# Kernel optimization log

Hardware: AMD Instinct MI355X
Metric: run time of the kernel (lower is better)

Reference implementation:

```python
import jax, jax.numpy as jnp
import numpy as np

B, N, NC, D, DC, L, NH = 8, 512, 256, 512, 256, 12, 8
DK = D // NH


def _ln(x, g, b, eps=1e-5):
    m = x.mean(-1, keepdims=True)
    v = ((x - m) ** 2).mean(-1, keepdims=True)
    return (x - m) * jax.lax.rsqrt(v + eps) * g + b


def setup_inputs() -> dict:
    key = jax.random.key(0)
    ks = iter(jax.random.split(key, 64))
    def rn(shape, s=1.0):
        return jax.random.normal(next(ks), shape, dtype=jnp.float32) * s
    w = 0.02
    inp = {
        "x_t": rn((B, N, 2)),
        "a_t": jax.random.uniform(next(ks), (B, N, N), dtype=jnp.float32),
        "hdse_node": rn((B, N, D), 0.1),
        "hdse_bias": rn((B, NH, N, N), 0.1),
        "context": rn((B, NC, DC)),
        "coord_w": rn((2, D), w), "coord_b": jnp.zeros((D,)),
        "deg_w": rn((1, D), w), "deg_b": jnp.zeros((D,)),
        "tm_w1": rn((D, 4 * D), w), "tm_b1": jnp.zeros((4 * D,)),
        "tm_w2": rn((4 * D, D), w), "tm_b2": jnp.zeros((D,)),
        "ln_sa_g": jnp.ones((L, D)), "ln_sa_b": jnp.zeros((L, D)),
        "qkv_w": rn((L, D, 3 * D), w), "qkv_b": jnp.zeros((L, 3 * D)),
        "osa_w": rn((L, D, D), w), "osa_b": jnp.zeros((L, D)),
        "ln_ca_g": jnp.ones((L, D)), "ln_ca_b": jnp.zeros((L, D)),
        "qca_w": rn((L, D, D), w), "qca_b": jnp.zeros((L, D)),
        "kvca_w": rn((L, DC, 2 * D), w), "kvca_b": jnp.zeros((L, 2 * D)),
        "oca_w": rn((L, D, D), w), "oca_b": jnp.zeros((L, D)),
        "ln_ff_g": jnp.ones((L, D)), "ln_ff_b": jnp.zeros((L, D)),
        "ff1_w": rn((L, D, 4 * D), w), "ff1_b": jnp.zeros((L, 4 * D)),
        "ff2_w": rn((L, 4 * D, D), w), "ff2_b": jnp.zeros((L, D)),
        "fn_g": jnp.ones((D,)), "fn_b": jnp.zeros((D,)),
        "ch_w": rn((D, 2), w), "ch_b": jnp.zeros((2,)),
        "es_w": rn((D, D // 4), w), "es_b": jnp.zeros((D // 4,)),
        "ed_w": rn((D, D // 4), w), "ed_b": jnp.zeros((D // 4,)),
        "eb": jnp.zeros((1,)),
        "t": jax.random.randint(next(ks), (B,), 0, 1000),
        "node_mask": jnp.ones((B, N), dtype=bool),
        "context_mask": jnp.ones((B, NC), dtype=bool),
    }
    return inp


def reference(x_t, a_t, hdse_node, hdse_bias, context,
              coord_w, coord_b, deg_w, deg_b,
              tm_w1, tm_b1, tm_w2, tm_b2,
              ln_sa_g, ln_sa_b, qkv_w, qkv_b, osa_w, osa_b,
              ln_ca_g, ln_ca_b, qca_w, qca_b, kvca_w, kvca_b, oca_w, oca_b,
              ln_ff_g, ln_ff_b, ff1_w, ff1_b, ff2_w, ff2_b,
              fn_g, fn_b, ch_w, ch_b, es_w, es_b, ed_w, ed_b, eb,
              t, node_mask, context_mask):
    scale = 1.0 / np.sqrt(DK).astype(np.float32)
    # input embedding: coords + degree + timestep + HDSE node encodings
    h = x_t @ coord_w + coord_b
    h = h + a_t.sum(-1, keepdims=True) @ deg_w + deg_b
    half = D // 2
    freqs = jnp.exp(-jnp.log(10000.0) * jnp.arange(half, dtype=jnp.float32) / half)
    ang = t.astype(jnp.float32)[:, None] * freqs[None, :]
    emb = jnp.concatenate([jnp.sin(ang), jnp.cos(ang)], -1)
    temb = jax.nn.gelu(emb @ tm_w1 + tm_b1, approximate=False) @ tm_w2 + tm_b2
    h = h + temb[:, None, :] + hdse_node
    nmask = node_mask[:, None, None, :]
    cmask = context_mask[:, None, None, :]
    for i in range(L):
        # self-attention with HDSE bias
        hn = _ln(h, ln_sa_g[i], ln_sa_b[i])
        qkv = (hn @ qkv_w[i] + qkv_b[i]).reshape(B, N, 3, NH, DK)
        q, k, v = [jnp.moveaxis(qkv[:, :, j], 1, 2) for j in range(3)]  # (B,NH,N,DK)
        s = jnp.einsum('bhnd,bhmd->bhnm', q, k) * scale + hdse_bias
        s = jnp.where(nmask, s, -1e9)
        sa = jnp.einsum('bhnm,bhmd->bhnd', jax.nn.softmax(s, -1), v)
        sa = jnp.moveaxis(sa, 1, 2).reshape(B, N, D)
        h = h + sa @ osa_w[i] + osa_b[i]
        # cross-attention to context
        hn = _ln(h, ln_ca_g[i], ln_ca_b[i])
        q = jnp.moveaxis((hn @ qca_w[i] + qca_b[i]).reshape(B, N, NH, DK), 1, 2)
        kv = (context @ kvca_w[i] + kvca_b[i]).reshape(B, NC, 2, NH, DK)
        kc = jnp.moveaxis(kv[:, :, 0], 1, 2)
        vc = jnp.moveaxis(kv[:, :, 1], 1, 2)
        s = jnp.einsum('bhnd,bhmd->bhnm', q, kc) * scale
        s = jnp.where(cmask, s, -1e9)
        ca = jnp.einsum('bhnm,bhmd->bhnd', jax.nn.softmax(s, -1), vc)
        ca = jnp.moveaxis(ca, 1, 2).reshape(B, N, D)
        h = h + ca @ oca_w[i] + oca_b[i]
        # FFN
        hn = _ln(h, ln_ff_g[i], ln_ff_b[i])
        h = h + jax.nn.gelu(hn @ ff1_w[i] + ff1_b[i], approximate=False) @ ff2_w[i] + ff2_b[i]
    h = _ln(h, fn_g, fn_b)
    eps = h @ ch_w + ch_b
    hs = h @ es_w + es_b
    hd = h @ ed_w + ed_b
    el = jnp.einsum('bne,bme->bnm', hs, hd) + eb[0]
    el = (el + jnp.swapaxes(el, 1, 2)) * 0.5
    el = jnp.where(jnp.eye(N, dtype=bool)[None], 0.0, el)
    eps = eps * node_mask[..., None].astype(eps.dtype)
    pm = node_mask[:, :, None] & node_mask[:, None, :]
    el = jnp.where(pm, el, 0.0)
    return eps, el
```

## Files before the change

### kernel.cpp

```cpp
#include <hip/hip_runtime.h>


#define DEV static __device__ __forceinline__

typedef __attribute__((ext_vector_type(8))) short short8;
typedef __attribute__((ext_vector_type(4))) short short4v;
typedef __attribute__((ext_vector_type(4))) float f32x4;

DEV float b2f(unsigned short u) {
    union { unsigned int i; float f; } x; x.i = ((unsigned int)u) << 16; return x.f;
}
DEV unsigned short f2b(float f) {
    union { float f; unsigned int i; } x; x.f = f;
    unsigned int i = x.i;
    return (unsigned short)((i + 0x7fffu + ((i >> 16) & 1u)) >> 16);
}
DEV float gelu_exact(float x) { return 0.5f * x * (1.0f + erff(x * 0.70710678118654752440f)); }

DEV void load_lds16(const unsigned short* g, unsigned short* l) {
    __builtin_amdgcn_global_load_lds(
        (const __attribute__((address_space(1))) unsigned int*)g,
        (__attribute__((address_space(3))) unsigned int*)l, 16, 0, 0);
}

template<int BM, int BN, int EPI>
__launch_bounds__(256)
__global__ void gemm_bt(const unsigned short* __restrict__ A, int lda, long sA1, long sA2,
                        const unsigned short* __restrict__ Bt, int ldb, long sB1, long sB2,
                        void* __restrict__ Cv, int ldc, long sC1, long sC2,
                        const float* __restrict__ bias,
                        int K, int NZ2)
{
    constexpr int WM = BM / 2, WN = BN / 2;
    constexpr int MF = WM / 16, NF = WN / 16;
    constexpr int LA = BM / 64, LB = BN / 64;
    __shared__ __align__(16) unsigned short lA0[BM * 32];
    __shared__ __align__(16) unsigned short lA1[BM * 32];
    __shared__ __align__(16) unsigned short lB0[BN * 32];
    __shared__ __align__(16) unsigned short lB1[BN * 32];

    const int tid = threadIdx.x;
    const int lane = tid & 63, wave = tid >> 6;
    const int quad = lane >> 4, l16 = lane & 15;
    const int wm = wave >> 1, wn = wave & 1;

    const int z = blockIdx.z;
    const int z1 = z / NZ2, z2 = z - z1 * NZ2;
    const unsigned short* Ab = A + z1 * sA1 + z2 * sA2 + (long)blockIdx.y * BM * lda;
    const unsigned short* Bb = Bt + z1 * sB1 + z2 * sB2 + (long)blockIdx.x * BN * ldb;

    const int srow = tid >> 2, scol = (tid & 3) * 8;

    f32x4 acc[MF][NF] = {};

    auto stage = [&](unsigned short* dA, unsigned short* dB, int k0) {
        #pragma unroll
        for (int i = 0; i < LA; i++)
            load_lds16(Ab + (long)(srow + i * 64) * lda + k0 + scol,
                       dA + (srow + i * 64) * 32 + scol);
        #pragma unroll
        for (int i = 0; i < LB; i++)
            load_lds16(Bb + (long)(srow + i * 64) * ldb + k0 + scol,
                       dB + (srow + i * 64) * 32 + scol);
    };
    auto compute = [&](const unsigned short* sA, const unsigned short* sB) {
        short8 af[MF], bf[NF];
        #pragma unroll
        for (int m = 0; m < MF; m++)
            af[m] = *(const short8*)&sA[(wm * WM + m * 16 + l16) * 32 + quad * 8];
        #pragma unroll
        for (int n = 0; n < NF; n++)
            bf[n] = *(const short8*)&sB[(wn * WN + n * 16 + l16) * 32 + quad * 8];
        #pragma unroll
        for (int m = 0; m < MF; m++)
            #pragma unroll
            for (int n = 0; n < NF; n++)
                acc[m][n] = __builtin_amdgcn_mfma_f32_16x16x32_bf16(af[m], bf[n], acc[m][n], 0, 0, 0);
    };

    const int nk = K >> 5;
    stage(lA0, lB0, 0);
    __syncthreads();

    for (int t = 0; t < nk; t += 2) {
        stage(lA1, lB1, (t + 1) << 5);
        compute(lA0, lB0);
        __syncthreads();
        if (t + 2 < nk) stage(lA0, lB0, (t + 2) << 5);
        compute(lA1, lB1);
        __syncthreads();
    }

    const long cb = z1 * sC1 + z2 * sC2;
    const int r0 = blockIdx.y * BM + wm * WM + quad * 4;
    const int c0 = blockIdx.x * BN + wn * WN + l16;
    #pragma unroll
    for (int m = 0; m < MF; m++) {
        #pragma unroll
        for (int n = 0; n < NF; n++) {
            const int c = c0 + n * 16;
            float bvv = 0.f;
            if (EPI == 0 || EPI == 1 || EPI == 2) bvv = bias ? bias[c] : 0.f;
            #pragma unroll
            for (int t2 = 0; t2 < 4; t2++) {
                const int r = r0 + m * 16 + t2;
                const float v = acc[m][n][t2];
                const long idx = cb + (long)r * ldc + c;
                if (EPI == 0) {
                    ((unsigned short*)Cv)[idx] = f2b(v + bvv);
                } else if (EPI == 1) {
                    ((unsigned short*)Cv)[idx] = f2b(gelu_exact(v + bvv));
                } else if (EPI == 2) {
                    float* Cf = (float*)Cv;
                    Cf[idx] = Cf[idx] + v + bvv;
                } else {
                    ((float*)Cv)[idx] = v;
                }
            }
        }
    }
}

template<int NKT, bool HB>
__launch_bounds__(256)
__global__ void attn_fused(const unsigned short* __restrict__ Qp, int ldq,
                           const unsigned short* __restrict__ Kp, int ldk,
                           const unsigned short* __restrict__ Vt,
                           const unsigned short* __restrict__ biasp,
                           unsigned short* __restrict__ Out)
{
    constexpr int KEYS = NKT * 128;
    __shared__ __align__(16) unsigned short kbuf[8192];
    __shared__ __align__(16) unsigned short vbuf[8192];
    __shared__ __align__(16) unsigned short pbuf[8192];

    const int tid = threadIdx.x;
    const int lane = tid & 63, w = tid >> 6;
    const int quad = lane >> 4, l16 = lane & 15;
    const int qblk = blockIdx.x;
    const int bh = blockIdx.y;
    const int b = bh >> 3, hh = bh & 7;

    const unsigned short* Q = Qp + (long)(b * 512 + qblk * 64) * ldq + hh * 64;
    const unsigned short* K = Kp + (long)b * KEYS * ldk + hh * 64;
    const unsigned short* V = Vt + (long)bh * 64 * KEYS;
    const unsigned short* Bi = HB ? biasp + (long)bh * 262144 + (long)(qblk * 64) * 512 : nullptr;
    unsigned short* O = Out + (long)(b * 512 + qblk * 64) * 512 + hh * 64;

    const short8 a0 = *(const short8*)(Q + (long)(w * 16 + l16) * ldq + quad * 8);
    const short8 a1 = *(const short8*)(Q + (long)(w * 16 + l16) * ldq + 32 + quad * 8);

    f32x4 acc[NKT * 8];
    #pragma unroll
    for (int f = 0; f < NKT * 8; f++) acc[f] = f32x4{0.f, 0.f, 0.f, 0.f};

    for (int kt = 0; kt < NKT; kt++) {
        __syncthreads();
        #pragma unroll
        for (int p = 0; p < 4; p++) {
            const int key = p * 32 + (tid >> 3);
            const int col = (tid & 7) * 8;
            short8 v = *(const short8*)(K + (long)(kt * 128 + key) * ldk + col);
            *(short8*)&kbuf[(col >> 5) * 4096 + key * 32 + (col & 31)] = v;
        }
        __syncthreads();
        #pragma unroll
        for (int nf = 0; nf < 8; nf++) {
            const short8 b0 = *(const short8*)&kbuf[(nf * 16 + l16) * 32 + quad * 8];
            const short8 b1 = *(const short8*)&kbuf[4096 + (nf * 16 + l16) * 32 + quad * 8];
            acc[kt * 8 + nf] = __builtin_amdgcn_mfma_f32_16x16x32_bf16(a0, b0, acc[kt * 8 + nf], 0, 0, 0);
            acc[kt * 8 + nf] = __builtin_amdgcn_mfma_f32_16x16x32_bf16(a1, b1, acc[kt * 8 + nf], 0, 0, 0);
        }
    }

    float rmax[4] = {-1e30f, -1e30f, -1e30f, -1e30f};
    #pragma unroll
    for (int f = 0; f < NKT * 8; f++) {
        const int col = (f >> 3) * 128 + (f & 7) * 16 + l16;
        #pragma unroll
        for (int j = 0; j < 4; j++) {
            float v = acc[f][j] * 0.125f;
            if (HB) v += b2f(Bi[(long)(w * 16 + quad * 4 + j) * 512 + col]);
            acc[f][j] = v;
            rmax[j] = fmaxf(rmax[j], v);
        }
    }
    #pragma unroll
    for (int m = 1; m < 16; m <<= 1)
        #pragma unroll
        for (int j = 0; j < 4; j++) rmax[j] = fmaxf(rmax[j], __shfl_xor(rmax[j], m, 64));
    float rsum[4] = {0.f, 0.f, 0.f, 0.f};
    #pragma unroll
    for (int f = 0; f < NKT * 8; f++)
        #pragma unroll
        for (int j = 0; j < 4; j++) {
            const float e = __expf(acc[f][j] - rmax[j]);
            acc[f][j] = e;
            rsum[j] += e;
        }
    #pragma unroll
    for (int m = 1; m < 16; m <<= 1)
        #pragma unroll
        for (int j = 0; j < 4; j++) rsum[j] += __shfl_xor(rsum[j], m, 64);
    float rinv[4];
    #pragma unroll
    for (int j = 0; j < 4; j++) rinv[j] = 1.f / rsum[j];

    f32x4 oacc[4];
    #pragma unroll
    for (int c = 0; c < 4; c++) oacc[c] = f32x4{0.f, 0.f, 0.f, 0.f};

    for (int kt = 0; kt < NKT; kt++) {
        __syncthreads();
        #pragma unroll
        for (int p = 0; p < 4; p++) {
            const int dk = p * 16 + (tid >> 4);
            const int keyloc = (tid & 15) * 8;
            short8 v = *(const short8*)(V + (long)dk * KEYS + kt * 128 + keyloc);
            *(short8*)&vbuf[(keyloc >> 5) * 2048 + dk * 32 + (keyloc & 31)] = v;
        }
        #pragma unroll
        for (int nf = 0; nf < 8; nf++) {
            const int keyloc = nf * 16 + l16;
            #pragma unroll
            for (int j = 0; j < 4; j++)
                pbuf[(keyloc >> 5) * 2048 + (w * 16 + quad * 4 + j) * 32 + (keyloc & 31)]
                    = f2b(acc[kt * 8 + nf][j] * rinv[j]);
        }
        __syncthreads();
        #pragma unroll
        for (int ks = 0; ks < 4; ks++) {
            const short8 ap = *(const short8*)&pbuf[ks * 2048 + (w * 16 + l16) * 32 + quad * 8];
            #pragma unroll
            for (int c = 0; c < 4; c++) {
                const short8 bp = *(const short8*)&vbuf[ks * 2048 + (c * 16 + l16) * 32 + quad * 8];
                oacc[c] = __builtin_amdgcn_mfma_f32_16x16x32_bf16(ap, bp, oacc[c], 0, 0, 0);
            }
        }
    }

    #pragma unroll
    for (int c = 0; c < 4; c++)
        #pragma unroll
        for (int j = 0; j < 4; j++)
            O[(long)(w * 16 + quad * 4 + j) * 512 + c * 16 + l16] = f2b(oacc[c][j]);
}

__launch_bounds__(256)
__global__ void ln_kernel(const float* __restrict__ x, const float* __restrict__ g,
                          const float* __restrict__ bb, unsigned short* __restrict__ out)
{
    const int lane = threadIdx.x & 63;
    const long row = (long)blockIdx.x * 4 + (threadIdx.x >> 6);
    const float* xr = x + row * 512 + lane * 8;
    float v[8];
    *(f32x4*)v = *(const f32x4*)xr;
    *(f32x4*)(v + 4) = *(const f32x4*)(xr + 4);
    float s = 0.f;
    #pragma unroll
    for (int j = 0; j < 8; j++) s += v[j];
    #pragma unroll
    for (int m = 1; m < 64; m <<= 1) s += __shfl_xor(s, m, 64);
    const float mean = s * (1.f / 512.f);
    float q = 0.f;
    #pragma unroll
    for (int j = 0; j < 8; j++) { float d = v[j] - mean; q += d * d; }
    #pragma unroll
    for (int m = 1; m < 64; m <<= 1) q += __shfl_xor(q, m, 64);
    const float rstd = rsqrtf(q * (1.f / 512.f) + 1e-5f);
    const int d0 = lane * 8;
    unsigned short o[8];
    #pragma unroll
    for (int j = 0; j < 8; j++) o[j] = f2b((v[j] - mean) * rstd * g[d0 + j] + bb[d0 + j]);
    *(short8*)(out + row * 512 + d0) = *(short8*)o;
}

__launch_bounds__(256)
__global__ void lnf_kernel(const float* __restrict__ x, const float* __restrict__ g,
                           const float* __restrict__ bb, float* __restrict__ out)
{
    const int lane = threadIdx.x & 63;
    const long row = (long)blockIdx.x * 4 + (threadIdx.x >> 6);
    const float* xr = x + row * 512 + lane * 8;
    float v[8];
    *(f32x4*)v = *(const f32x4*)xr;
    *(f32x4*)(v + 4) = *(const f32x4*)(xr + 4);
    float s = 0.f;
    #pragma unroll
    for (int j = 0; j < 8; j++) s += v[j];
    #pragma unroll
    for (int m = 1; m < 64; m <<= 1) s += __shfl_xor(s, m, 64);
    const float mean = s * (1.f / 512.f);
    float q = 0.f;
    #pragma unroll
    for (int j = 0; j < 8; j++) { float d = v[j] - mean; q += d * d; }
    #pragma unroll
    for (int m = 1; m < 64; m <<= 1) q += __shfl_xor(q, m, 64);
    const float rstd = rsqrtf(q * (1.f / 512.f) + 1e-5f);
    const int d0 = lane * 8;
    float o[8];
    #pragma unroll
    for (int j = 0; j < 8; j++) o[j] = (v[j] - mean) * rstd * g[d0 + j] + bb[d0 + j];
    *(f32x4*)(out + row * 512 + d0) = *(const f32x4*)o;
    *(f32x4*)(out + row * 512 + d0 + 4) = *(const f32x4*)(o + 4);
}

__global__ void wtrans(const float* __restrict__ W, unsigned short* __restrict__ WT, int K, int Nc)
{
    __shared__ float tile[32][33];
    const long zoff = (long)blockIdx.z * K * Nc;
    const int c0 = blockIdx.x * 32, k0 = blockIdx.y * 32;
    const int tx = threadIdx.x, ty = threadIdx.y;
    const float* Wz = W + zoff;
    unsigned short* WTz = WT + zoff;
    #pragma unroll
    for (int i = 0; i < 4; i++)
        tile[ty + i * 8][tx] = Wz[(long)(k0 + ty + i * 8) * Nc + c0 + tx];
    __syncthreads();
    #pragma unroll
    for (int i = 0; i < 4; i++)
        WTz[(long)(c0 + ty + i * 8) * K + k0 + tx] = f2b(tile[tx][ty + i * 8]);
}

__global__ void transp(const unsigned short* __restrict__ src, unsigned short* __restrict__ dst,
                       int ldin, int R, long sS1, long sS2, int NZ2, long sDz)
{
    __shared__ unsigned short tile[32][33];
    const int z = blockIdx.z;
    const unsigned short* s = src + (long)(z / NZ2) * sS1 + (long)(z % NZ2) * sS2;
    unsigned short* d = dst + (long)z * sDz;
    const int r0 = blockIdx.x * 32, c0 = blockIdx.y * 32;
    const int tx = threadIdx.x, ty = threadIdx.y;
    #pragma unroll
    for (int i = 0; i < 4; i++)
        tile[ty + i * 8][tx] = s[(long)(r0 + ty + i * 8) * ldin + c0 + tx];
    __syncthreads();
    #pragma unroll
    for (int i = 0; i < 4; i++)
        d[(long)(c0 + ty + i * 8) * R + r0 + tx] = tile[tx][ty + i * 8];
}

__launch_bounds__(256)
__global__ void cast_kernel(const float* __restrict__ in, unsigned short* __restrict__ out, long n4)
{
    const long i = (long)blockIdx.x * 256 + threadIdx.x;
    if (i >= n4) return;
    const f32x4 v = *(const f32x4*)(in + i * 4);
    unsigned short o[4] = { f2b(v.x), f2b(v.y), f2b(v.z), f2b(v.w) };
    *(short4v*)(out + i * 4) = *(short4v*)o;
}

__launch_bounds__(256)
__global__ void rowsum_kernel(const float* __restrict__ a, float* __restrict__ out)
{
    const int lane = threadIdx.x & 63;
    const long row = (long)blockIdx.x * 4 + (threadIdx.x >> 6);
    const float* ar = a + row * 512 + lane * 8;
    const f32x4 v0 = *(const f32x4*)ar, v1 = *(const f32x4*)(ar + 4);
    float s = v0.x + v0.y + v0.z + v0.w + v1.x + v1.y + v1.z + v1.w;
    #pragma unroll
    for (int m = 1; m < 64; m <<= 1) s += __shfl_xor(s, m, 64);
    if (lane == 0) out[row] = s;
}

__launch_bounds__(256)
__global__ void temb1_kernel(const int* __restrict__ t, const unsigned short* __restrict__ w1t,
                             const float* __restrict__ b1, unsigned short* __restrict__ hid)
{
    __shared__ float emb[512];
    const int b = blockIdx.x >> 3, cb = blockIdx.x & 7, tid = threadIdx.x;
    {
        const float fr = expf(-9.21034037197618f * (float)tid * (1.f / 256.f));
        const float ang = (float)t[b] * fr;
        emb[tid] = sinf(ang);
        emb[tid + 256] = cosf(ang);
    }
    __syncthreads();
    const int o = cb * 256 + tid;
    const unsigned short* wr = w1t + (long)o * 512;
    float acc = b1[o];
    for (int k = 0; k < 512; k += 8) {
        unsigned short u[8];
        *(short8*)u = *(const short8*)(wr + k);
        #pragma unroll
        for (int j = 0; j < 8; j++) acc += emb[k + j] * b2f(u[j]);
    }
    hid[b * 2048 + o] = f2b(gelu_exact(acc));
}

__launch_bounds__(256)
__global__ void temb2_kernel(const unsigned short* __restrict__ hid, const unsigned short* __restrict__ w2t,
                             const float* __restrict__ b2, float* __restrict__ temb)
{
    const int b = blockIdx.x >> 1;
    const int o = (blockIdx.x & 1) * 256 + threadIdx.x;
    const unsigned short* hr = hid + b * 2048;
    const unsigned short* wr = w2t + (long)o * 2048;
    float acc = b2[o];
    for (int k = 0; k < 2048; k += 8) {
        unsigned short hu[8], wu[8];
        *(short8*)hu = *(const short8*)(hr + k);
        *(short8*)wu = *(const short8*)(wr + k);
        #pragma unroll
        for (int j = 0; j < 8; j++) acc += b2f(hu[j]) * b2f(wu[j]);
    }
    temb[b * 512 + o] = acc;
}

__launch_bounds__(256)
__global__ void embed_kernel(const float* __restrict__ x_t, const float* __restrict__ deg,
                             const float* __restrict__ coord_w, const float* __restrict__ coord_b,
                             const float* __restrict__ deg_w, const float* __restrict__ deg_b,
                             const float* __restrict__ temb, const float* __restrict__ hdse_node,
                             float* __restrict__ h)
{
    const long i = (long)blockIdx.x * 256 + threadIdx.x;
    const int d = (int)(i & 511);
    const long row = i >> 9;
    const int b = (int)(row >> 9);
    h[i] = x_t[row * 2] * coord_w[d] + x_t[row * 2 + 1] * coord_w[512 + d] + coord_b[d]
         + deg[row] * deg_w[d] + deg_b[d] + temb[b * 512 + d] + hdse_node[i];
}

__launch_bounds__(256)
__global__ void epsf_kernel(const float* __restrict__ hnf, const float* __restrict__ ch_w,
                            const float* __restrict__ ch_b, float* __restrict__ out)
{
    const int lane = threadIdx.x & 63;
    const long row = (long)blockIdx.x * 4 + (threadIdx.x >> 6);
    const float* hr = hnf + row * 512 + lane * 8;
    float v[8];
    *(f32x4*)v = *(const f32x4*)hr;
    *(f32x4*)(v + 4) = *(const f32x4*)(hr + 4);
    float e0 = 0.f, e1 = 0.f;
    const int d0 = lane * 8;
    #pragma unroll
    for (int j = 0; j < 8; j++) {
        e0 += v[j] * ch_w[(d0 + j) * 2];
        e1 += v[j] * ch_w[(d0 + j) * 2 + 1];
    }
    #pragma unroll
    for (int m = 1; m < 64; m <<= 1) { e0 += __shfl_xor(e0, m, 64); e1 += __shfl_xor(e1, m, 64); }
    if (lane == 0) { out[row * 2] = e0 + ch_b[0]; out[row * 2 + 1] = e1 + ch_b[1]; }
}

__launch_bounds__(256)
__global__ void headw_kernel(const float* __restrict__ hnf, const float* __restrict__ W,
                             const float* __restrict__ bias, float* __restrict__ out)
{
    __shared__ __align__(16) float rows[8][512];
    const long r0 = (long)blockIdx.x * 8;
    const int tid = threadIdx.x;
    #pragma unroll
    for (int i = 0; i < 4; i++) {
        const int idx = tid + i * 256;
        *(f32x4*)&rows[idx >> 7][(idx & 127) * 4] = *(const f32x4*)(hnf + r0 * 512 + (long)idx * 4);
    }
    __syncthreads();
    const int r = tid >> 5, cg = (tid & 31) * 4;
    f32x4 acc = *(const f32x4*)(bias + cg);
    #pragma unroll 4
    for (int k = 0; k < 512; k++) {
        const f32x4 wv = *(const f32x4*)(W + (long)k * 128 + cg);
        const float a = rows[r][k];
        acc.x += a * wv.x; acc.y += a * wv.y; acc.z += a * wv.z; acc.w += a * wv.w;
    }
    *(f32x4*)(out + (r0 + r) * 128 + cg) = acc;
}

__launch_bounds__(256)
__global__ void el_kernel(const float* __restrict__ hs, const float* __restrict__ hd,
                          float* __restrict__ el)
{
    __shared__ float sA[32 * 129];
    __shared__ __align__(16) float sB[128 * 36];
    const int b = blockIdx.z;
    const int n0 = blockIdx.y * 32, m0 = blockIdx.x * 32;
    const float* hsb = hs + ((long)b * 512 + n0) * 128;
    const float* hdb = hd + ((long)b * 512 + m0) * 128;
    const int tid = threadIdx.x;
    const int lr = tid >> 3, lc = (tid & 7) * 16;
    #pragma unroll
    for (int j = 0; j < 4; j++) {
        const f32x4 av = *(const f32x4*)(hsb + (long)lr * 128 + lc + j * 4);
        const f32x4 bv = *(const f32x4*)(hdb + (long)lr * 128 + lc + j * 4);
        #pragma unroll
        for (int u = 0; u < 4; u++) {
            sA[lr * 129 + lc + j * 4 + u] = av[u];
            sB[(lc + j * 4 + u) * 36 + lr] = bv[u];
        }
    }
    __syncthreads();
    const int n = tid >> 3, m = (tid & 7) * 4;
    float a0 = 0.f, a1 = 0.f, a2 = 0.f, a3 = 0.f;
    #pragma unroll 4
    for (int k = 0; k < 128; k++) {
        const float a = sA[n * 129 + k];
        const f32x4 bv = *(const f32x4*)&sB[k * 36 + m];
        a0 += a * bv.x; a1 += a * bv.y; a2 += a * bv.z; a3 += a * bv.w;
    }
    float* o = el + ((long)b * 512 + n0 + n) * 512 + m0 + m;
    const f32x4 r = {a0, a1, a2, a3};
    *(f32x4*)o = r;
}

__launch_bounds__(256)
__global__ void sym_kernel(const float* __restrict__ elb, const float* __restrict__ eb,
                           float* __restrict__ out)
{
    const long i = (long)blockIdx.x * 256 + threadIdx.x;
    const int m = (int)(i & 511);
    const long t = i >> 9;
    const int n = (int)(t & 511);
    const int b = (int)(t >> 9);
    const long base = (long)b * 262144;
    out[i] = (n == m) ? 0.f
           : 0.5f * (elb[base + (long)n * 512 + m] + elb[base + (long)m * 512 + n]) + eb[0];
}

extern "C" void kernel_launch(void* const* d_in, const int* in_sizes, int n_in,
                              void* d_out, int out_size, void* d_ws, size_t ws_size,
                              hipStream_t stream)
{
    const float* x_t       = (const float*)d_in[0];
    const float* a_t       = (const float*)d_in[1];
    const float* hdse_node = (const float*)d_in[2];
    const float* hdse_bias = (const float*)d_in[3];
    const float* context   = (const float*)d_in[4];
    const float* coord_w   = (const float*)d_in[5];
    const float* coord_b   = (const float*)d_in[6];
    const float* deg_w     = (const float*)d_in[7];
    const float* deg_b     = (const float*)d_in[8];
    const float* tm_w1     = (const float*)d_in[9];
    const float* tm_b1     = (const float*)d_in[10];
    const float* tm_w2     = (const float*)d_in[11];
    const float* tm_b2     = (const float*)d_in[12];
    const float* ln_sa_g   = (const float*)d_in[13];
    const float* ln_sa_b   = (const float*)d_in[14];
    const float* qkv_w     = (const float*)d_in[15];
    const float* qkv_b     = (const float*)d_in[16];
    const float* osa_w     = (const float*)d_in[17];
    const float* osa_b     = (const float*)d_in[18];
    const float* ln_ca_g   = (const float*)d_in[19];
    const float* ln_ca_b   = (const float*)d_in[20];
    const float* qca_w     = (const float*)d_in[21];
    const float* qca_b     = (const float*)d_in[22];
    const float* kvca_w    = (const float*)d_in[23];
    const float* kvca_b    = (const float*)d_in[24];
    const float* oca_w     = (const float*)d_in[25];
    const float* oca_b     = (const float*)d_in[26];
    const float* ln_ff_g   = (const float*)d_in[27];
    const float* ln_ff_b   = (const float*)d_in[28];
    const float* ff1_w     = (const float*)d_in[29];
    const float* ff1_b     = (const float*)d_in[30];
    const float* ff2_w     = (const float*)d_in[31];
    const float* ff2_b     = (const float*)d_in[32];
    const float* fn_g      = (const float*)d_in[33];
    const float* fn_b      = (const float*)d_in[34];
    const float* ch_w      = (const float*)d_in[35];
    const float* ch_b      = (const float*)d_in[36];
    const float* es_w      = (const float*)d_in[37];
    const float* es_b      = (const float*)d_in[38];
    const float* ed_w      = (const float*)d_in[39];
    const float* ed_b      = (const float*)d_in[40];
    const float* eb        = (const float*)d_in[41];
    const int*   tt        = (const int*)d_in[42];

    char* w = (char*)d_ws;
    size_t off = 0;
    auto alloc = [&](size_t bytes) -> void* {
        void* p = w + off;
        off = (off + bytes + 255) & ~(size_t)255;
        return p;
    };

    unsigned short* qkv_wt  = (unsigned short*)alloc(12UL * 1536 * 512 * 2);
    unsigned short* osa_wt  = (unsigned short*)alloc(12UL * 512 * 512 * 2);
    unsigned short* qca_wt  = (unsigned short*)alloc(12UL * 512 * 512 * 2);
    unsigned short* kvca_wt = (unsigned short*)alloc(12UL * 1024 * 256 * 2);
    unsigned short* oca_wt  = (unsigned short*)alloc(12UL * 512 * 512 * 2);
    unsigned short* ff1_wt  = (unsigned short*)alloc(12UL * 2048 * 512 * 2);
    unsigned short* ff2_wt  = (unsigned short*)alloc(12UL * 512 * 2048 * 2);
    unsigned short* tm1t    = (unsigned short*)alloc(2048UL * 512 * 2);
    unsigned short* tm2t    = (unsigned short*)alloc(512UL * 2048 * 2);
    unsigned short* biasb   = (unsigned short*)alloc(16777216UL * 2);
    unsigned short* ctxb    = (unsigned short*)alloc(524288UL * 2);
    float*          h     = (float*)alloc(4096UL * 512 * 4);
    unsigned short* hn    = (unsigned short*)alloc(4096UL * 512 * 2);
    float*          hnf   = (float*)alloc(4096UL * 512 * 4);
    unsigned short* qkvb  = (unsigned short*)alloc(4096UL * 1536 * 2);
    unsigned short* vt    = (unsigned short*)alloc(64UL * 64 * 512 * 2);
    unsigned short* vtc   = (unsigned short*)alloc(64UL * 64 * 256 * 2);
    unsigned short* attn  = (unsigned short*)alloc(4096UL * 512 * 2);
    unsigned short* qcab  = (unsigned short*)alloc(4096UL * 512 * 2);
    unsigned short* kvb   = (unsigned short*)alloc(2048UL * 1024 * 2);
    unsigned short* ffb   = (unsigned short*)alloc(4096UL * 2048 * 2);
    float*          hsf   = (float*)alloc(4096UL * 128 * 4);
    float*          hdf   = (float*)alloc(4096UL * 128 * 4);
    float*          elbuf = (float*)alloc(8UL * 512 * 512 * 4);
    float*          degb  = (float*)alloc(4096UL * 4);
    unsigned short* thid  = (unsigned short*)alloc(8UL * 2048 * 2);
    float*          tembb = (float*)alloc(8UL * 512 * 4);

    if (off > ws_size) return;

    const dim3 tb(32, 8);

    wtrans<<<dim3(48, 16, 12), tb, 0, stream>>>(qkv_w,  qkv_wt,  512, 1536);
    wtrans<<<dim3(16, 16, 12), tb, 0, stream>>>(osa_w,  osa_wt,  512, 512);
    wtrans<<<dim3(16, 16, 12), tb, 0, stream>>>(qca_w,  qca_wt,  512, 512);
    wtrans<<<dim3(32,  8, 12), tb, 0, stream>>>(kvca_w, kvca_wt, 256, 1024);
    wtrans<<<dim3(16, 16, 12), tb, 0, stream>>>(oca_w,  oca_wt,  512, 512);
    wtrans<<<dim3(64, 16, 12), tb, 0, stream>>>(ff1_w,  ff1_wt,  512, 2048);
    wtrans<<<dim3(16, 64, 12), tb, 0, stream>>>(ff2_w,  ff2_wt,  2048, 512);
    wtrans<<<dim3(64, 16, 1),  tb, 0, stream>>>(tm_w1,  tm1t,    512, 2048);
    wtrans<<<dim3(16, 64, 1),  tb, 0, stream>>>(tm_w2,  tm2t,    2048, 512);
    cast_kernel<<<16384, 256, 0, stream>>>(hdse_bias, biasb, 4194304L);
    cast_kernel<<<512, 256, 0, stream>>>(context, ctxb, 131072L);

    rowsum_kernel<<<1024, 256, 0, stream>>>(a_t, degb);
    temb1_kernel<<<64, 256, 0, stream>>>(tt, tm1t, tm_b1, thid);
    temb2_kernel<<<16, 256, 0, stream>>>(thid, tm2t, tm_b2, tembb);
    embed_kernel<<<8192, 256, 0, stream>>>(x_t, degb, coord_w, coord_b, deg_w, deg_b,
                                           tembb, hdse_node, h);

    for (int l = 0; l < 12; l++) {
        const unsigned short* qkvW  = qkv_wt  + (size_t)l * 1536 * 512;
        const unsigned short* osaW  = osa_wt  + (size_t)l * 512 * 512;
        const unsigned short* qcaW  = qca_wt  + (size_t)l * 512 * 512;
        const unsigned short* kvcaW = kvca_wt + (size_t)l * 1024 * 256;
        const unsigned short* ocaW  = oca_wt  + (size_t)l * 512 * 512;
        const unsigned short* ff1W  = ff1_wt  + (size_t)l * 2048 * 512;
        const unsigned short* ff2W  = ff2_wt  + (size_t)l * 512 * 2048;

        ln_kernel<<<1024, 256, 0, stream>>>(h, ln_sa_g + l * 512, ln_sa_b + l * 512, hn);
        gemm_bt<128, 128, 0><<<dim3(12, 32, 1), 256, 0, stream>>>(
            hn, 512, 0, 0, qkvW, 512, 0, 0, qkvb, 1536, 0, 0,
            qkv_b + l * 1536, 512, 1);
        transp<<<dim3(16, 2, 64), tb, 0, stream>>>(qkvb + 1024, vt, 1536, 512,
                                                   786432L, 64L, 8, 32768L);
        attn_fused<4, true><<<dim3(8, 64), 256, 0, stream>>>(
            qkvb, 1536, qkvb + 512, 1536, vt, biasb, attn);
        gemm_bt<64, 128, 2><<<dim3(4, 64, 1), 256, 0, stream>>>(
            attn, 512, 0, 0, osaW, 512, 0, 0, h, 512, 0, 0,
            osa_b + l * 512, 512, 1);

        ln_kernel<<<1024, 256, 0, stream>>>(h, ln_ca_g + l * 512, ln_ca_b + l * 512, hn);
        gemm_bt<64, 128, 0><<<dim3(4, 64, 1), 256, 0, stream>>>(
            hn, 512, 0, 0, qcaW, 512, 0, 0, qcab, 512, 0, 0,
            qca_b + l * 512, 512, 1);
        gemm_bt<64, 128, 0><<<dim3(8, 32, 1), 256, 0, stream>>>(
            ctxb, 256, 0, 0, kvcaW, 256, 0, 0, kvb, 1024, 0, 0,
            kvca_b + l * 1024, 256, 1);
        transp<<<dim3(8, 2, 64), tb, 0, stream>>>(kvb + 512, vtc, 1024, 256,
                                                  262144L, 64L, 8, 16384L);
        attn_fused<2, false><<<dim3(8, 64), 256, 0, stream>>>(
            qcab, 512, kvb, 1024, vtc, nullptr, attn);
        gemm_bt<64, 128, 2><<<dim3(4, 64, 1), 256, 0, stream>>>(
            attn, 512, 0, 0, ocaW, 512, 0, 0, h, 512, 0, 0,
            oca_b + l * 512, 512, 1);

        ln_kernel<<<1024, 256, 0, stream>>>(h, ln_ff_g + l * 512, ln_ff_b + l * 512, hn);
        gemm_bt<128, 128, 1><<<dim3(16, 32, 1), 256, 0, stream>>>(
            hn, 512, 0, 0, ff1W, 512, 0, 0, ffb, 2048, 0, 0,
            ff1_b + l * 2048, 512, 1);
        gemm_bt<64, 128, 2><<<dim3(4, 64, 1), 256, 0, stream>>>(
            ffb, 2048, 0, 0, ff2W, 2048, 0, 0, h, 512, 0, 0,
            ff2_b + l * 512, 2048, 1);
    }

    lnf_kernel<<<1024, 256, 0, stream>>>(h, fn_g, fn_b, hnf);
    epsf_kernel<<<1024, 256, 0, stream>>>(hnf, ch_w, ch_b, (float*)d_out);
    headw_kernel<<<512, 256, 0, stream>>>(hnf, es_w, es_b, hsf);
    headw_kernel<<<512, 256, 0, stream>>>(hnf, ed_w, ed_b, hdf);
    el_kernel<<<dim3(16, 16, 8), 256, 0, stream>>>(hsf, hdf, elbuf);
    sym_kernel<<<8192, 256, 0, stream>>>(elbuf, eb, (float*)d_out + 8192);
}
```

Baseline: 2.932 ms.

## Deepen GEMM LDS prefetch with explicit vmcnt waits and fuse head projections

The bf16 GEMM now issues two K-tiles of async global-to-LDS loads up front. Each step waits on vmcnt counters and raw s_barriers instead of full __syncthreads, so the load for tile t+2 overlaps the MFMAs of tile t. Separately, the two final head projections (es/ed) are merged into one kernel that reads each hidden row once, splits K across half-waves and combines the halves with a shuffle. The hand-written waitcnt values depend on the exact number of outstanding loads per thread, which is fragile if tile shapes change.

```diff
diff --git a/kernel.cpp b/kernel.cpp
--- a/kernel.cpp
+++ b/kernel.cpp
@@ -22,6 +22,9 @@
         (const __attribute__((address_space(1))) unsigned int*)g,
         (__attribute__((address_space(3))) unsigned int*)l, 16, 0, 0);
 }
+
+#define S_VMCNT(n) asm volatile("s_waitcnt vmcnt(" #n ")" ::: "memory")
+#define S_LGKMCNT0 asm volatile("s_waitcnt lgkmcnt(0)" ::: "memory")
 
 template<int BM, int BN, int EPI>
 __launch_bounds__(256)
@@ -34,6 +37,7 @@
     constexpr int WM = BM / 2, WN = BN / 2;
     constexpr int MF = WM / 16, NF = WN / 16;
     constexpr int LA = BM / 64, LB = BN / 64;
+    constexpr int L = LA + LB;
     __shared__ __align__(16) unsigned short lA0[BM * 32];
     __shared__ __align__(16) unsigned short lA1[BM * 32];
     __shared__ __align__(16) unsigned short lB0[BN * 32];
@@ -63,14 +67,27 @@
             load_lds16(Bb + (long)(srow + i * 64) * ldb + k0 + scol,
                        dB + (srow + i * 64) * 32 + scol);
     };
-    auto compute = [&](const unsigned short* sA, const unsigned short* sB) {
+
+    const int nk = K >> 5;
+    stage(lA0, lB0, 0);
+    stage(lA1, lB1, 32);
+
+    auto step = [&](int t, unsigned short* cA, unsigned short* cB) {
+        if (t + 1 < nk) { if constexpr (L == 3) S_VMCNT(3); else S_VMCNT(4); }
+        else            S_VMCNT(0);
+        __builtin_amdgcn_s_barrier();
+        __builtin_amdgcn_sched_barrier(0);
         short8 af[MF], bf[NF];
         #pragma unroll
         for (int m = 0; m < MF; m++)
-            af[m] = *(const short8*)&sA[(wm * WM + m * 16 + l16) * 32 + quad * 8];
+            af[m] = *(const short8*)&cA[(wm * WM + m * 16 + l16) * 32 + quad * 8];
         #pragma unroll
         for (int n = 0; n < NF; n++)
-            bf[n] = *(const short8*)&sB[(wn * WN + n * 16 + l16) * 32 + quad * 8];
+            bf[n] = *(const short8*)&cB[(wn * WN + n * 16 + l16) * 32 + quad * 8];
+        S_LGKMCNT0;
+        __builtin_amdgcn_s_barrier();
+        __builtin_amdgcn_sched_barrier(0);
+        if (t + 2 < nk) stage(cA, cB, (t + 2) << 5);
         #pragma unroll
         for (int m = 0; m < MF; m++)
             #pragma unroll
@@ -78,17 +95,9 @@
                 acc[m][n] = __builtin_amdgcn_mfma_f32_16x16x32_bf16(af[m], bf[n], acc[m][n], 0, 0, 0);
     };
 
-    const int nk = K >> 5;
-    stage(lA0, lB0, 0);
-    __syncthreads();
-
     for (int t = 0; t < nk; t += 2) {
-        stage(lA1, lB1, (t + 1) << 5);
-        compute(lA0, lB0);
-        __syncthreads();
-        if (t + 2 < nk) stage(lA0, lB0, (t + 2) << 5);
-        compute(lA1, lB1);
-        __syncthreads();
+        step(t,     lA0, lB0);
+        step(t + 1, lA1, lB1);
     }
 
     const long cb = z1 * sC1 + z2 * sC2;
@@ -445,27 +454,49 @@
 }
 
 __launch_bounds__(256)
-__global__ void headw_kernel(const float* __restrict__ hnf, const float* __restrict__ W,
-                             const float* __restrict__ bias, float* __restrict__ out)
-{
-    __shared__ __align__(16) float rows[8][512];
-    const long r0 = (long)blockIdx.x * 8;
+__global__ void headw2_kernel(const float* __restrict__ hnf,
+                              const float* __restrict__ We, const float* __restrict__ be,
+                              const float* __restrict__ Wd, const float* __restrict__ bd,
+                              float* __restrict__ oe, float* __restrict__ od)
+{
+    __shared__ __align__(16) float rows[4][512];
+    const long r0 = (long)blockIdx.x * 4;
     const int tid = threadIdx.x;
     #pragma unroll
-    for (int i = 0; i < 4; i++) {
+    for (int i = 0; i < 2; i++) {
         const int idx = tid + i * 256;
         *(f32x4*)&rows[idx >> 7][(idx & 127) * 4] = *(const f32x4*)(hnf + r0 * 512 + (long)idx * 4);
     }
     __syncthreads();
-    const int r = tid >> 5, cg = (tid & 31) * 4;
-    f32x4 acc = *(const f32x4*)(bias + cg);
+    const int row = tid >> 6;
+    const int lane = tid & 63;
+    const int kh = lane >> 5;
+    const int cg = (lane & 31) * 4;
+    const float* rw = &rows[row][kh * 256];
+    const float* pe = We + (long)(kh * 256) * 128 + cg;
+    const float* pd = Wd + (long)(kh * 256) * 128 + cg;
+    f32x4 ae = {0.f, 0.f, 0.f, 0.f}, ad = {0.f, 0.f, 0.f, 0.f};
     #pragma unroll 4
-    for (int k = 0; k < 512; k++) {
-        const f32x4 wv = *(const f32x4*)(W + (long)k * 128 + cg);
-        const float a = rows[r][k];
-        acc.x += a * wv.x; acc.y += a * wv.y; acc.z += a * wv.z; acc.w += a * wv.w;
-    }
-    *(f32x4*)(out + (r0 + r) * 128 + cg) = acc;
+    for (int k = 0; k < 256; k++) {
+        const float a = rw[k];
+        const f32x4 we = *(const f32x4*)(pe + (long)k * 128);
+        const f32x4 wd = *(const f32x4*)(pd + (long)k * 128);
+        ae.x += a * we.x; ae.y += a * we.y; ae.z += a * we.z; ae.w += a * we.w;
+        ad.x += a * wd.x; ad.y += a * wd.y; ad.z += a * wd.z; ad.w += a * wd.w;
+    }
+    #pragma unroll
+    for (int c = 0; c < 4; c++) {
+        ae[c] += __shfl_xor(ae[c], 32, 64);
+        ad[c] += __shfl_xor(ad[c], 32, 64);
+    }
+    if (kh == 0) {
+        const f32x4 bve = *(const f32x4*)(be + cg);
+        const f32x4 bvd = *(const f32x4*)(bd + cg);
+        const f32x4 re = {ae.x + bve.x, ae.y + bve.y, ae.z + bve.z, ae.w + bve.w};
+        const f32x4 rd = {ad.x + bvd.x, ad.y + bvd.y, ad.z + bvd.z, ad.w + bvd.w};
+        *(f32x4*)(oe + (r0 + row) * 128 + cg) = re;
+        *(f32x4*)(od + (r0 + row) * 128 + cg) = rd;
+    }
 }
 
 __launch_bounds__(256)
@@ -671,8 +702,7 @@
 
     lnf_kernel<<<1024, 256, 0, stream>>>(h, fn_g, fn_b, hnf);
     epsf_kernel<<<1024, 256, 0, stream>>>(hnf, ch_w, ch_b, (float*)d_out);
-    headw_kernel<<<512, 256, 0, stream>>>(hnf, es_w, es_b, hsf);
-    headw_kernel<<<512, 256, 0, stream>>>(hnf, ed_w, ed_b, hdf);
+    headw2_kernel<<<1024, 256, 0, stream>>>(hnf, es_w, es_b, ed_w, ed_b, hsf, hdf);
     el_kernel<<<dim3(16, 16, 8), 256, 0, stream>>>(hsf, hdf, elbuf);
     sym_kernel<<<8192, 256, 0, stream>>>(elbuf, eb, (float*)d_out + 8192);
 }
```

Measured after the change: 2.778 ms. 1.06x faster.
